# Performance work log

Measured on AMD Instinct MI355X. Metric: run time of the kernel, lower is better.

Reference implementation:

```python
import jax, jax.numpy as jnp
import numpy as np

MIN_BW = 0.1
MAX_BW = 10.0
BW_FACTOR = 1.0
SAMPLE = 512  # min(512, B) with B >= 512


def _pairwise_dist_sq(a, b):
    # ||a_i - b_j||^2 via GEMM: [N, M], avoids [N, M, D] intermediate
    a2 = jnp.sum(a * a, axis=-1)[:, None]
    b2 = jnp.sum(b * b, axis=-1)[None, :]
    d = a2 + b2 - 2.0 * (a @ b.T)
    return jnp.maximum(d, 0.0)


def _bandwidth(x, y):
    # torch: median heuristic on first SAMPLE rows, under no_grad
    xs = jax.lax.stop_gradient(x[:SAMPLE])
    ys = jax.lax.stop_gradient(y[:SAMPLE])
    dist_sq = _pairwise_dist_sq(xs, ys)
    bw_sq = jnp.median(dist_sq.reshape(-1))
    bw = jnp.sqrt(bw_sq / 2.0) * BW_FACTOR
    return jnp.clip(bw, MIN_BW, MAX_BW)


def setup_inputs() -> dict:
    key = jax.random.key(0)
    kx, ksx, ky, ksy = jax.random.split(key, 4)
    B, D = 4096, 512
    return {
        "x": jax.random.normal(kx, (B, D), dtype=jnp.float32),
        "score_x": jax.random.normal(ksx, (B, D), dtype=jnp.float32),
        "y": jax.random.normal(ky, (B, D), dtype=jnp.float32),
        "score_y": jax.random.normal(ksy, (B, D), dtype=jnp.float32),
    }


def reference(x, score_x, y, score_y):
    D = x.shape[-1]
    h = _bandwidth(x, y)
    h2 = h * h

    dist_sq = _pairwise_dist_sq(x, y)                      # [B, B]
    k = jnp.exp(-dist_sq / (2.0 * h2))                     # [B, B]

    # term1[i,j] = k[i,j] * <score_x_i, score_y_j>
    term1 = k * (score_x @ score_y.T)

    # term2[i,j] = <x_i - y_j, score_y_j> * k[i,j] / h^2
    term2 = ((x @ score_y.T) - jnp.sum(y * score_y, axis=-1)[None, :]) * k / h2

    # term3[i,j] = ||x_i - y_j||^2 * k / h^4 - k * D / h^2
    term3 = dist_sq * k / (h2 * h2) - k * (D / h2)

    return term1 + term2 + term3
```

## Files before the change

kernel.cpp:

```cpp
#include <hip/hip_runtime.h>
#include <hip/hip_bf16.h>

typedef __attribute__((ext_vector_type(8))) short bf16x8;
typedef __attribute__((ext_vector_type(4))) float f32x4;

#define B_N 4096
#define DIM 512
#define HBINS 8192

#define OFF_PARAMS 0
#define OFF_X2     256
#define OFF_Y2     16640
#define OFF_YSY    33024
#define OFF_HIST   49408
#define OFF_TILES  98304
#define MAT_ELEMS  2097152
#define WS_NEED    (OFF_TILES + (size_t)4 * MAT_ELEMS * 2)

static __device__ __forceinline__ unsigned short f2bf_rne(float f) {
    unsigned int u = __float_as_uint(f);
    u += 0x7FFFu + ((u >> 16) & 1u);
    return (unsigned short)(u >> 16);
}
static __device__ __forceinline__ float bf2f(unsigned short h) {
    return __uint_as_float(((unsigned int)h) << 16);
}

static __device__ __forceinline__ int swz(int r, int k) {
    return r * 32 + ((((k >> 3) ^ ((r >> 1) & 3))) << 3) + (k & 7);
}

__global__ __launch_bounds__(256) void k_hist2(
    const float* __restrict__ X, const float* __restrict__ Y,
    unsigned int* __restrict__ hist) {
    __shared__ __align__(16) unsigned short sA[2048];
    __shared__ __align__(16) unsigned short sB[2048];
    __shared__ unsigned int hloc[HBINS];
    __shared__ float x2s[64], y2s[64];

    int t = threadIdx.x;
    int bi = blockIdx.y, bj = blockIdx.x;
    for (int i = t; i < HBINS; i += 256) hloc[i] = 0;

    int lane = t & 63, w = t >> 6;
    int wm = w >> 1, wn = w & 1;
    int fr = lane & 15, fko = (lane >> 4) * 8;

    f32x4 axy[2][2];
#pragma unroll
    for (int i = 0; i < 2; ++i)
#pragma unroll
        for (int j = 0; j < 2; ++j) axy[i][j] = (f32x4)0.f;

    int r = t >> 2, k0 = (t & 3) * 8;
    const float* gx = X + (size_t)(bi * 64 + r) * DIM + k0;
    const float* gy = Y + (size_t)(bj * 64 + r) * DIM + k0;

    int ixA[2], ixB[2];
#pragma unroll
    for (int fm = 0; fm < 2; ++fm) ixA[fm] = swz(wm * 32 + fm * 16 + fr, fko);
#pragma unroll
    for (int fn = 0; fn < 2; ++fn) ixB[fn] = swz(wn * 32 + fn * 16 + fr, fko);

    float na = 0.f, nb = 0.f;
    float4 A0, A1, B0, B1;
#define LDK(kt_) do {                                                       \
        A0 = *(const float4*)(gx + (kt_) * 32);                             \
        A1 = *(const float4*)(gx + (kt_) * 32 + 4);                         \
        B0 = *(const float4*)(gy + (kt_) * 32);                             \
        B1 = *(const float4*)(gy + (kt_) * 32 + 4);                         \
    } while (0)

    LDK(0);
    for (int kt = 0; kt < 16; ++kt) {
        float av[8] = {A0.x, A0.y, A0.z, A0.w, A1.x, A1.y, A1.z, A1.w};
        float bv[8] = {B0.x, B0.y, B0.z, B0.w, B1.x, B1.y, B1.z, B1.w};
        bf16x8 ha, hb;
#pragma unroll
        for (int j = 0; j < 8; ++j) {
            na += av[j] * av[j];
            nb += bv[j] * bv[j];
            ha[j] = (short)f2bf_rne(av[j]);
            hb[j] = (short)f2bf_rne(bv[j]);
        }
        __syncthreads();
        *(bf16x8*)&sA[swz(r, k0)] = ha;
        *(bf16x8*)&sB[swz(r, k0)] = hb;
        if (kt < 15) LDK(kt + 1);
        __syncthreads();

        bf16x8 aX[2];
#pragma unroll
        for (int fm = 0; fm < 2; ++fm) aX[fm] = *(const bf16x8*)&sA[ixA[fm]];
#pragma unroll
        for (int fn = 0; fn < 2; ++fn) {
            bf16x8 bY = *(const bf16x8*)&sB[ixB[fn]];
#pragma unroll
            for (int fm = 0; fm < 2; ++fm)
                axy[fm][fn] = __builtin_amdgcn_mfma_f32_16x16x32_bf16(aX[fm], bY, axy[fm][fn], 0, 0, 0);
        }
    }
#undef LDK

    na += __shfl_xor(na, 1); na += __shfl_xor(na, 2);
    nb += __shfl_xor(nb, 1); nb += __shfl_xor(nb, 2);
    if ((t & 3) == 0) { x2s[r] = na; y2s[r] = nb; }
    __syncthreads();

    int fq = lane >> 4;
#pragma unroll
    for (int fm = 0; fm < 2; ++fm)
#pragma unroll
        for (int fn = 0; fn < 2; ++fn)
#pragma unroll
            for (int rr = 0; rr < 4; ++rr) {
                int rl = wm * 32 + fm * 16 + fq * 4 + rr;
                int cl = wn * 32 + fn * 16 + fr;
                float d = fmaxf(x2s[rl] + y2s[cl] - 2.0f * axy[fm][fn][rr], 0.0f);
                int bin = (int)(d * 4.0f);
                if (bin > HBINS - 1) bin = HBINS - 1;
                atomicAdd(&hloc[bin], 1u);
            }
    __syncthreads();
    for (int i = t; i < HBINS; i += 256) {
        unsigned int v = hloc[i];
        if (v) atomicAdd(&hist[i], v);
    }
}

__global__ __launch_bounds__(256, 1) void k_median(
    const unsigned int* __restrict__ hist, float* __restrict__ params) {
    __shared__ unsigned int hsum[HBINS];
    __shared__ unsigned int part[256];
    __shared__ float vv[2];
    int t = threadIdx.x;
    for (int i = t; i < HBINS / 4; i += 256)
        ((uint4*)hsum)[i] = ((const uint4*)hist)[i];
    __syncthreads();
    unsigned int s = 0;
#pragma unroll 8
    for (int b = t * 32; b < t * 32 + 32; ++b) s += hsum[b];
    part[t] = s;
    __syncthreads();
    unsigned int pre = 0;
    for (int i = 0; i < 256; ++i) {
        unsigned int v = part[i];
        if (i < t) pre += v;
    }
    const unsigned int kk1 = 131072u, kk2 = 131073u;
    unsigned int hi = pre + s;
#pragma unroll
    for (int sel = 0; sel < 2; ++sel) {
        unsigned int kk = sel ? kk2 : kk1;
        if (kk > pre && kk <= hi) {
            unsigned int cc = pre;
            for (int b = 0; b < 32; ++b) {
                cc += hsum[t * 32 + b];
                if (cc >= kk) { vv[sel] = ((float)(t * 32 + b) + 0.5f) * 0.25f; break; }
            }
        }
    }
    __syncthreads();
    if (t == 0) {
        float med = 0.5f * (vv[0] + vv[1]);
        float bw = sqrtf(med * 0.5f);
        bw = fminf(fmaxf(bw, 0.1f), 10.0f);
        float h2 = bw * bw;
        params[0] = 1.0f / (2.0f * h2);
        params[1] = 1.0f / h2;
        params[2] = 1.0f / (h2 * h2);
        params[3] = (float)DIM / h2;
    }
}

__global__ void k_prestats(const float* __restrict__ X, const float* __restrict__ SX,
                           const float* __restrict__ Y, const float* __restrict__ SY,
                           const float* __restrict__ params, unsigned short* __restrict__ tiles,
                           float* __restrict__ x2, float* __restrict__ y2,
                           float* __restrict__ ysy) {
    int side = blockIdx.z;
    const float* P = side ? Y : X;
    const float* Q = side ? SY : SX;
    float c1 = side ? 0.0f : params[1];
    int tile = blockIdx.x, t = threadIdx.x;
    unsigned short* base0 = tiles + (size_t)side * 2 * MAT_ELEMS;
    unsigned short* base1 = base0 + MAT_ELEMS;

#pragma unroll
    for (int kt2 = 0; kt2 < 2; ++kt2) {
        int kt = blockIdx.y * 2 + kt2;
        unsigned short* d0 = base0 + (size_t)(tile * 16 + kt) * 4096;
        unsigned short* d1 = base1 + (size_t)(tile * 16 + kt) * 4096;

#pragma unroll
        for (int c = 0; c < 2; ++c) {
            int u = c * 256 + t;
            int r = u >> 2;
            int k = (((u & 3) ^ ((u >> 3) & 3))) << 3;
            const float* gp = P + (size_t)(tile * 128 + r) * DIM + kt * 32 + k;
            float4 p0 = *(const float4*)gp;
            float4 p1 = *(const float4*)(gp + 4);
            float pv[8] = {p0.x, p0.y, p0.z, p0.w, p1.x, p1.y, p1.z, p1.w};
            float s1 = 0.f, s2 = 0.f;
            bf16x8 h0;
            if (side) {
                const float* gq = Q + (size_t)(tile * 128 + r) * DIM + kt * 32 + k;
                float4 q0 = *(const float4*)gq;
                float4 q1 = *(const float4*)(gq + 4);
                float qv[8] = {q0.x, q0.y, q0.z, q0.w, q1.x, q1.y, q1.z, q1.w};
#pragma unroll
                for (int j = 0; j < 8; ++j) {
                    s1 += pv[j] * pv[j];
                    s2 += pv[j] * qv[j];
                    h0[j] = (short)f2bf_rne(pv[j]);
                }
            } else {
#pragma unroll
                for (int j = 0; j < 8; ++j) {
                    s1 += pv[j] * pv[j];
                    h0[j] = (short)f2bf_rne(pv[j]);
                }
            }
            *(bf16x8*)&d0[u * 8] = h0;
            s1 += __shfl_xor(s1, 1); s1 += __shfl_xor(s1, 2);
            if (side) { s2 += __shfl_xor(s2, 1); s2 += __shfl_xor(s2, 2); }
            if ((t & 3) == 0) {
                int row = tile * 128 + r;
                if (side == 0) {
                    atomicAdd(&x2[row], s1);
                } else {
                    atomicAdd(&y2[row], s1);
                    atomicAdd(&ysy[row], s2);
                }
            }
        }

#pragma unroll
        for (int c = 0; c < 2; ++c) {
            int v = c * 256 + t;
            int r = (v >> 6) * 16 + (v & 15);
            int k = ((v >> 4) & 3) << 3;
            const float* gq = Q + (size_t)(tile * 128 + r) * DIM + kt * 32 + k;
            float4 q0 = *(const float4*)gq;
            float4 q1 = *(const float4*)(gq + 4);
            float qv[8] = {q0.x, q0.y, q0.z, q0.w, q1.x, q1.y, q1.z, q1.w};
            bf16x8 h1;
            if (side == 0) {
                const float* gp = P + (size_t)(tile * 128 + r) * DIM + kt * 32 + k;
                float4 p0 = *(const float4*)gp;
                float4 p1 = *(const float4*)(gp + 4);
                float pv[8] = {p0.x, p0.y, p0.z, p0.w, p1.x, p1.y, p1.z, p1.w};
#pragma unroll
                for (int j = 0; j < 8; ++j) h1[j] = (short)f2bf_rne(qv[j] + c1 * pv[j]);
            } else {
#pragma unroll
                for (int j = 0; j < 8; ++j) h1[j] = (short)f2bf_rne(qv[j]);
            }
            *(bf16x8*)&d1[v * 8] = h1;
        }
    }
}

#define GLD(g, l) __builtin_amdgcn_global_load_lds(                                   \
    (const __attribute__((address_space(1))) void*)(g),                               \
    (__attribute__((address_space(3))) void*)(l), 16, 0, 0)

__global__ __launch_bounds__(256, 2) void k_main(
    const unsigned short* __restrict__ tiles,
    const float* __restrict__ x2g, const float* __restrict__ y2g,
    const float* __restrict__ ysyg, const float* __restrict__ params,
    float* __restrict__ out) {
    __shared__ __align__(16) unsigned short sA[2][4096];
    __shared__ __align__(16) unsigned short sB[2][4096];
    __shared__ float x2s[128], y2s[128], ysys[128];

    int t = threadIdx.x;
    int bm = blockIdx.y, bn = blockIdx.x;
    if (t < 128) x2s[t] = x2g[bm * 128 + t];
    else { y2s[t - 128] = y2g[bn * 128 + (t - 128)]; ysys[t - 128] = ysyg[bn * 128 + (t - 128)]; }
    __syncthreads();

    int lane = t & 63, w = t >> 6;
    int wm = w >> 1, wn = w & 1;
    int fr = lane & 15, fko = (lane >> 4) * 8;

    f32x4 axy[4][4], acb[4][4];
#pragma unroll
    for (int i = 0; i < 4; ++i)
#pragma unroll
        for (int j = 0; j < 4; ++j) { axy[i][j] = (f32x4)0.f; acb[i][j] = (f32x4)0.f; }

    const unsigned short* gaX = tiles + (size_t)(bm * 16) * 4096 + t * 8;
    const unsigned short* gbY = tiles + (size_t)2 * MAT_ELEMS + (size_t)(bn * 16) * 4096 + t * 8;
    const unsigned short* gaC = tiles + (size_t)MAT_ELEMS + (size_t)(bm * 16) * 4096
                              + (wm * 4) * 512 + lane * 8;
    const unsigned short* gbS = tiles + (size_t)3 * MAT_ELEMS + (size_t)(bn * 16) * 4096
                              + (wn * 4) * 512 + lane * 8;

#define STAGE(buf, kt_) do {                                                     \
        const unsigned short* pa_ = gaX + (size_t)(kt_) * 4096;                  \
        const unsigned short* pb_ = gbY + (size_t)(kt_) * 4096;                  \
        GLD(pa_,        &sA[buf][t * 8]);                                        \
        GLD(pa_ + 2048, &sA[buf][2048 + t * 8]);                                 \
        GLD(pb_,        &sB[buf][t * 8]);                                        \
        GLD(pb_ + 2048, &sB[buf][2048 + t * 8]);                                 \
    } while (0)

#define FRAGLD(dC, dS, kt_) do {                                                 \
        const unsigned short* pc_ = gaC + (size_t)(kt_) * 4096;                  \
        const unsigned short* ps_ = gbS + (size_t)(kt_) * 4096;                  \
        dC[0] = *(const bf16x8*)(pc_);        dS[0] = *(const bf16x8*)(ps_);     \
        dC[1] = *(const bf16x8*)(pc_ + 512);  dS[1] = *(const bf16x8*)(ps_ + 512);\
        dC[2] = *(const bf16x8*)(pc_ + 1024); dS[2] = *(const bf16x8*)(ps_ + 1024);\
        dC[3] = *(const bf16x8*)(pc_ + 1536); dS[3] = *(const bf16x8*)(ps_ + 1536);\
    } while (0)

    int ixA[4], ixB[4];
#pragma unroll
    for (int fm = 0; fm < 4; ++fm) ixA[fm] = swz(wm * 64 + fm * 16 + fr, fko);
#pragma unroll
    for (int fn = 0; fn < 4; ++fn) ixB[fn] = swz(wn * 64 + fn * 16 + fr, fko);

    bf16x8 fC0[4], fS0[4], fC1[4], fS1[4];

#define KSTEP(CB, CURC, CURS, NXTC, NXTS, NKT, DOPF) do {                        \
        asm volatile("s_waitcnt vmcnt(8)" ::: "memory");   \
        __builtin_amdgcn_sched_barrier(0);                                       \
        __builtin_amdgcn_s_barrier();                                            \
        __builtin_amdgcn_sched_barrier(0);                                       \
        if (DOPF) {                                                              \
            STAGE(CB ^ 1, NKT);                                                  \
            FRAGLD(NXTC, NXTS, NKT);                                             \
        }                                                                        \
        bf16x8 dX[4], dY[4];                                                     \
        dX[0] = *(const bf16x8*)&sA[CB][ixA[0]];                                 \
        dX[1] = *(const bf16x8*)&sA[CB][ixA[1]];                                 \
        dX[2] = *(const bf16x8*)&sA[CB][ixA[2]];                                 \
        dX[3] = *(const bf16x8*)&sA[CB][ixA[3]];                                 \
        dY[0] = *(const bf16x8*)&sB[CB][ixB[0]];                                 \
        dY[1] = *(const bf16x8*)&sB[CB][ixB[1]];                                 \
        dY[2] = *(const bf16x8*)&sB[CB][ixB[2]];                                 \
        dY[3] = *(const bf16x8*)&sB[CB][ixB[3]];                                 \
        __builtin_amdgcn_s_setprio(1);                                           \
        _Pragma("unroll")                                                        \
        for (int fn_ = 0; fn_ < 4; ++fn_) {                                      \
            _Pragma("unroll")                                                    \
            for (int fm_ = 0; fm_ < 4; ++fm_) {                                  \
                axy[fm_][fn_] = __builtin_amdgcn_mfma_f32_16x16x32_bf16(         \
                    dX[fm_], dY[fn_], axy[fm_][fn_], 0, 0, 0);                   \
                acb[fm_][fn_] = __builtin_amdgcn_mfma_f32_16x16x32_bf16(         \
                    CURC[fm_], CURS[fn_], acb[fm_][fn_], 0, 0, 0);               \
            }                                                                    \
        }                                                                        \
        __builtin_amdgcn_s_setprio(0);                                           \
        __builtin_amdgcn_sched_barrier(0);                                       \
    } while (0)

    STAGE(0, 0);
    FRAGLD(fC0, fS0, 0);

    for (int k2 = 0; k2 < 7; ++k2) {
        KSTEP(0, fC0, fS0, fC1, fS1, 2 * k2 + 1, 1);
        KSTEP(1, fC1, fS1, fC0, fS0, 2 * k2 + 2, 1);
    }
    KSTEP(0, fC0, fS0, fC1, fS1, 15, 1);
    KSTEP(1, fC1, fS1, fC0, fS0, 0, 0);
#undef KSTEP
#undef STAGE
#undef FRAGLD

    float c0 = params[0], c1 = params[1], c2 = params[2], c3 = params[3];
    int fq = lane >> 4;
#pragma unroll
    for (int fm = 0; fm < 4; ++fm) {
#pragma unroll
        for (int fn = 0; fn < 4; ++fn) {
#pragma unroll
            for (int r = 0; r < 4; ++r) {
                int rl = wm * 64 + fm * 16 + fq * 4 + r;
                int cl = wn * 64 + fn * 16 + fr;
                float d = fmaxf(x2s[rl] + y2s[cl] - 2.0f * axy[fm][fn][r], 0.0f);
                float kv = __expf(-d * c0);
                out[(size_t)(bm * 128 + rl) * B_N + (bn * 128 + cl)] =
                    kv * (acb[fm][fn][r] - c1 * ysys[cl] + d * c2 - c3);
            }
        }
    }
}

__global__ void k_rowstats(const float* __restrict__ X, const float* __restrict__ Y,
                           const float* __restrict__ SY,
                           float* __restrict__ x2, float* __restrict__ y2,
                           float* __restrict__ ysy) {
    int t = threadIdx.x;
    int r = blockIdx.x * 4 + (t >> 6);
    int lane = t & 63;
    const float4* px = (const float4*)(X + (size_t)r * DIM) + lane * 2;
    const float4* py = (const float4*)(Y + (size_t)r * DIM) + lane * 2;
    const float4* ps = (const float4*)(SY + (size_t)r * DIM) + lane * 2;
    float4 a0 = px[0], a1 = px[1];
    float4 b0 = py[0], b1 = py[1];
    float4 c0 = ps[0], c1 = ps[1];
    float s1 = a0.x*a0.x + a0.y*a0.y + a0.z*a0.z + a0.w*a0.w
             + a1.x*a1.x + a1.y*a1.y + a1.z*a1.z + a1.w*a1.w;
    float s2 = b0.x*b0.x + b0.y*b0.y + b0.z*b0.z + b0.w*b0.w
             + b1.x*b1.x + b1.y*b1.y + b1.z*b1.z + b1.w*b1.w;
    float s3 = b0.x*c0.x + b0.y*c0.y + b0.z*c0.z + b0.w*c0.w
             + b1.x*c1.x + b1.y*c1.y + b1.z*c1.z + b1.w*c1.w;
#pragma unroll
    for (int o = 32; o > 0; o >>= 1) {
        s1 += __shfl_down(s1, o);
        s2 += __shfl_down(s2, o);
        s3 += __shfl_down(s3, o);
    }
    if (lane == 0) { x2[r] = s1; y2[r] = s2; ysy[r] = s3; }
}

__global__ void k_hist_fp32(const float* __restrict__ X, const float* __restrict__ Y,
                            const float* __restrict__ x2, const float* __restrict__ y2,
                            unsigned int* __restrict__ hist) {
    __shared__ float xs[32][68];
    __shared__ float ys[32][68];
    __shared__ unsigned int hloc[HBINS];
    int t = threadIdx.x;
    for (int i = t; i < HBINS; i += 256) hloc[i] = 0;
    int i0 = blockIdx.y * 32, j0 = blockIdx.x * 32;
    float a00 = 0.f, a01 = 0.f, a10 = 0.f, a11 = 0.f;
    int ti = (t >> 4) * 2, tj = (t & 15) * 2;
    for (int c = 0; c < 8; ++c) {
        __syncthreads();
        int rr = t >> 3, cc = (t & 7) * 8;
        const float* gx = X + (size_t)(i0 + rr) * DIM + c * 64 + cc;
        *(float4*)&xs[rr][cc] = *(const float4*)gx;
        *(float4*)&xs[rr][cc + 4] = *(const float4*)(gx + 4);
        const float* gy = Y + (size_t)(j0 + rr) * DIM + c * 64 + cc;
        *(float4*)&ys[rr][cc] = *(const float4*)gy;
        *(float4*)&ys[rr][cc + 4] = *(const float4*)(gy + 4);
        __syncthreads();
        for (int kk = 0; kk < 64; ++kk) {
            float a0 = xs[ti][kk], a1 = xs[ti + 1][kk];
            float b0 = ys[tj][kk], b1 = ys[tj + 1][kk];
            a00 += a0 * b0; a01 += a0 * b1; a10 += a1 * b0; a11 += a1 * b1;
        }
    }
    float s[2][2] = {{a00, a01}, {a10, a11}};
#pragma unroll
    for (int ii = 0; ii < 2; ++ii)
#pragma unroll
        for (int jj = 0; jj < 2; ++jj) {
            float d = fmaxf(x2[i0 + ti + ii] + y2[j0 + tj + jj] - 2.f * s[ii][jj], 0.f);
            int bin = (int)(d * 4.0f);
            if (bin > HBINS - 1) bin = HBINS - 1;
            atomicAdd(&hloc[bin], 1u);
        }
    __syncthreads();
    for (int i = t; i < HBINS; i += 256) {
        unsigned int v = hloc[i];
        if (v) atomicAdd(&hist[i], v);
    }
}

static __device__ __forceinline__ void store_hi(unsigned short* tile, int r, int k0,
                                                float4 v0, float4 v1) {
    bf16x8 h;
    h[0] = (short)f2bf_rne(v0.x); h[1] = (short)f2bf_rne(v0.y);
    h[2] = (short)f2bf_rne(v0.z); h[3] = (short)f2bf_rne(v0.w);
    h[4] = (short)f2bf_rne(v1.x); h[5] = (short)f2bf_rne(v1.y);
    h[6] = (short)f2bf_rne(v1.z); h[7] = (short)f2bf_rne(v1.w);
    *(bf16x8*)&tile[swz(r, k0)] = h;
}
static __device__ __forceinline__ void store_hilo(unsigned short* th, unsigned short* tl,
                                                  int r, int k0, float4 v0, float4 v1) {
    float f[8] = {v0.x, v0.y, v0.z, v0.w, v1.x, v1.y, v1.z, v1.w};
    bf16x8 h, l;
#pragma unroll
    for (int j = 0; j < 8; ++j) {
        unsigned short hh = f2bf_rne(f[j]);
        h[j] = (short)hh;
        l[j] = (short)f2bf_rne(f[j] - bf2f(hh));
    }
    *(bf16x8*)&th[swz(r, k0)] = h;
    *(bf16x8*)&tl[swz(r, k0)] = l;
}

__global__ __launch_bounds__(256, 2) void k_main_fb(
    const float* __restrict__ X, const float* __restrict__ SX,
    const float* __restrict__ Y, const float* __restrict__ SY,
    const float* __restrict__ x2g, const float* __restrict__ y2g,
    const float* __restrict__ ysyg, const float* __restrict__ params,
    float* __restrict__ out) {
    __shared__ __align__(16) unsigned short tX[4096];
    __shared__ __align__(16) unsigned short tSXH[4096];
    __shared__ __align__(16) unsigned short tSXL[4096];
    __shared__ __align__(16) unsigned short tY[2048];
    __shared__ __align__(16) unsigned short tSYH[2048];
    __shared__ __align__(16) unsigned short tSYL[2048];
    __shared__ float x2s[128];
    __shared__ float y2s[64];
    __shared__ float ysys[64];

    int t = threadIdx.x;
    int bm = blockIdx.y, bn = blockIdx.x;
    if (t < 128) x2s[t] = x2g[bm * 128 + t];
    else if (t < 192) y2s[t - 128] = y2g[bn * 64 + (t - 128)];
    else ysys[t - 192] = ysyg[bn * 64 + (t - 192)];

    int lane = t & 63, w = t >> 6, wm = w >> 1, wn = w & 1;
    f32x4 axy[4][2], ass[4][2], axsy[4][2];
#pragma unroll
    for (int i = 0; i < 4; ++i)
#pragma unroll
        for (int j = 0; j < 2; ++j) {
            axy[i][j] = (f32x4)0.f; ass[i][j] = (f32x4)0.f; axsy[i][j] = (f32x4)0.f;
        }

    for (int kt = 0; kt < DIM / 32; ++kt) {
        int kb = kt * 32;
#pragma unroll
        for (int h = 0; h < 2; ++h) {
            int s = t + h * 256;
            int r = s >> 2, k0 = (s & 3) * 8;
            const float* gx = X + (size_t)(bm * 128 + r) * DIM + kb + k0;
            store_hi(tX, r, k0, *(const float4*)gx, *(const float4*)(gx + 4));
            const float* gs = SX + (size_t)(bm * 128 + r) * DIM + kb + k0;
            store_hilo(tSXH, tSXL, r, k0, *(const float4*)gs, *(const float4*)(gs + 4));
        }
        {
            int r = t >> 2, k0 = (t & 3) * 8;
            const float* gy = Y + (size_t)(bn * 64 + r) * DIM + kb + k0;
            store_hi(tY, r, k0, *(const float4*)gy, *(const float4*)(gy + 4));
            const float* gq = SY + (size_t)(bn * 64 + r) * DIM + kb + k0;
            store_hilo(tSYH, tSYL, r, k0, *(const float4*)gq, *(const float4*)(gq + 4));
        }
        __syncthreads();

        int fr = lane & 15, fk = (lane >> 4) * 8;
        bf16x8 aX[4], aSH[4], aSL[4];
#pragma unroll
        for (int fm = 0; fm < 4; ++fm) {
            int ix = swz(wm * 64 + fm * 16 + fr, fk);
            aX[fm] = *(const bf16x8*)&tX[ix];
            aSH[fm] = *(const bf16x8*)&tSXH[ix];
            aSL[fm] = *(const bf16x8*)&tSXL[ix];
        }
#pragma unroll
        for (int fn = 0; fn < 2; ++fn) {
            int iy = swz(wn * 32 + fn * 16 + fr, fk);
            bf16x8 bY = *(const bf16x8*)&tY[iy];
            bf16x8 bH = *(const bf16x8*)&tSYH[iy];
            bf16x8 bL = *(const bf16x8*)&tSYL[iy];
#pragma unroll
            for (int fm = 0; fm < 4; ++fm) {
                axy[fm][fn] = __builtin_amdgcn_mfma_f32_16x16x32_bf16(aX[fm], bY, axy[fm][fn], 0, 0, 0);
                ass[fm][fn] = __builtin_amdgcn_mfma_f32_16x16x32_bf16(aSH[fm], bH, ass[fm][fn], 0, 0, 0);
                ass[fm][fn] = __builtin_amdgcn_mfma_f32_16x16x32_bf16(aSH[fm], bL, ass[fm][fn], 0, 0, 0);
                ass[fm][fn] = __builtin_amdgcn_mfma_f32_16x16x32_bf16(aSL[fm], bH, ass[fm][fn], 0, 0, 0);
                axsy[fm][fn] = __builtin_amdgcn_mfma_f32_16x16x32_bf16(aX[fm], bH, axsy[fm][fn], 0, 0, 0);
            }
        }
        __syncthreads();
    }

    float c0 = params[0], c1 = params[1], c2 = params[2], c3 = params[3];
    int fr = lane & 15, fq = lane >> 4;
#pragma unroll
    for (int fm = 0; fm < 4; ++fm)
#pragma unroll
        for (int fn = 0; fn < 2; ++fn)
#pragma unroll
            for (int r = 0; r < 4; ++r) {
                int rl = wm * 64 + fm * 16 + fq * 4 + r;
                int cl = wn * 32 + fn * 16 + fr;
                float d = fmaxf(x2s[rl] + y2s[cl] - 2.0f * axy[fm][fn][r], 0.0f);
                float kv = __expf(-d * c0);
                out[(size_t)(bm * 128 + rl) * B_N + (bn * 64 + cl)] =
                    kv * ass[fm][fn][r] + (axsy[fm][fn][r] - ysys[cl]) * (kv * c1)
                    + d * kv * c2 - kv * c3;
            }
}

extern "C" void kernel_launch(void* const* d_in, const int* in_sizes, int n_in,
                              void* d_out, int out_size, void* d_ws, size_t ws_size,
                              hipStream_t stream) {
    const float* x  = (const float*)d_in[0];
    const float* sx = (const float*)d_in[1];
    const float* y  = (const float*)d_in[2];
    const float* sy = (const float*)d_in[3];
    float* out = (float*)d_out;
    char* ws = (char*)d_ws;
    float* params = (float*)(ws + OFF_PARAMS);
    float* x2 = (float*)(ws + OFF_X2);
    float* y2 = (float*)(ws + OFF_Y2);
    float* ysy = (float*)(ws + OFF_YSY);
    unsigned int* hist = (unsigned int*)(ws + OFF_HIST);
    unsigned short* tiles = (unsigned short*)(ws + OFF_TILES);

    if (ws_size >= WS_NEED) {
        hipMemsetAsync(ws + OFF_X2, 0, 3 * 16384 + HBINS * 4, stream);
        k_hist2<<<dim3(8, 8), dim3(256), 0, stream>>>(x, y, hist);
        k_median<<<1, 256, 0, stream>>>(hist, params);
        k_prestats<<<dim3(32, 8, 2), dim3(256), 0, stream>>>(x, sx, y, sy, params, tiles,
                                                             x2, y2, ysy);
        k_main<<<dim3(32, 32), dim3(256), 0, stream>>>(tiles, x2, y2, ysy, params, out);
    } else {
        hipMemsetAsync(hist, 0, HBINS * 4, stream);
        k_rowstats<<<B_N / 4, 256, 0, stream>>>(x, y, sy, x2, y2, ysy);
        k_hist_fp32<<<dim3(16, 16), dim3(256), 0, stream>>>(x, y, x2, y2, hist);
        k_median<<<1, 256, 0, stream>>>(hist, params);
        k_main_fb<<<dim3(64, 32), dim3(256), 0, stream>>>(x, sx, y, sy, x2, y2, ysy, params, out);
    }
}
```

Baseline: 85.48 us.

## Merge histogram, median and param-independent preprocessing into one kernel

Folds the histogram kernel, the median kernel and the param-independent part of the tile preprocessing (bf16 conversion of X, Y and SY plus row norms) into a single 576-block launch. The last block to finish, detected with an atomic counter, computes the median. Only the param-dependent SX+c1*X tile conversion stays in a small separate kernel. Tile storage moves to a fragment-linear layout, so the main kernel uses plain lane*8 offsets instead of swizzled indices. This removes two launches and lets the preprocessing run alongside the histogram, at the cost of a threadfence/counter tail and uneven block work.

New measurement: 146.8 us. 71.7% more time.

```diff
diff --git a/kernel.cpp b/kernel.cpp
--- a/kernel.cpp
+++ b/kernel.cpp
@@ -13,9 +13,11 @@
 #define OFF_Y2     16640
 #define OFF_YSY    33024
 #define OFF_HIST   49408
+#define OFF_CNT    82176
 #define OFF_TILES  98304
 #define MAT_ELEMS  2097152
 #define WS_NEED    (OFF_TILES + (size_t)4 * MAT_ELEMS * 2)
+#define MEMSET_LEN 82180
 
 static __device__ __forceinline__ unsigned short f2bf_rne(float f) {
     unsigned int u = __float_as_uint(f);
@@ -30,232 +32,246 @@
     return r * 32 + ((((k >> 3) ^ ((r >> 1) & 3))) << 3) + (k & 7);
 }
 
-__global__ __launch_bounds__(256) void k_hist2(
+
+__global__ __launch_bounds__(256) void k_pre1(
     const float* __restrict__ X, const float* __restrict__ Y,
-    unsigned int* __restrict__ hist) {
-    __shared__ __align__(16) unsigned short sA[2048];
-    __shared__ __align__(16) unsigned short sB[2048];
+    const float* __restrict__ SY, unsigned short* __restrict__ tiles,
+    float* __restrict__ x2, float* __restrict__ y2, float* __restrict__ ysy,
+    unsigned int* __restrict__ hist, unsigned int* __restrict__ cnt,
+    float* __restrict__ params) {
+    __shared__ __align__(16) unsigned short sAB[4096];
     __shared__ unsigned int hloc[HBINS];
-    __shared__ float x2s[64], y2s[64];
-
-    int t = threadIdx.x;
-    int bi = blockIdx.y, bj = blockIdx.x;
-    for (int i = t; i < HBINS; i += 256) hloc[i] = 0;
-
-    int lane = t & 63, w = t >> 6;
-    int wm = w >> 1, wn = w & 1;
-    int fr = lane & 15, fko = (lane >> 4) * 8;
-
-    f32x4 axy[2][2];
-#pragma unroll
-    for (int i = 0; i < 2; ++i)
-#pragma unroll
-        for (int j = 0; j < 2; ++j) axy[i][j] = (f32x4)0.f;
-
-    int r = t >> 2, k0 = (t & 3) * 8;
-    const float* gx = X + (size_t)(bi * 64 + r) * DIM + k0;
-    const float* gy = Y + (size_t)(bj * 64 + r) * DIM + k0;
-
-    int ixA[2], ixB[2];
-#pragma unroll
-    for (int fm = 0; fm < 2; ++fm) ixA[fm] = swz(wm * 32 + fm * 16 + fr, fko);
-#pragma unroll
-    for (int fn = 0; fn < 2; ++fn) ixB[fn] = swz(wn * 32 + fn * 16 + fr, fko);
-
-    float na = 0.f, nb = 0.f;
-    float4 A0, A1, B0, B1;
-#define LDK(kt_) do {                                                       \
-        A0 = *(const float4*)(gx + (kt_) * 32);                             \
-        A1 = *(const float4*)(gx + (kt_) * 32 + 4);                         \
-        B0 = *(const float4*)(gy + (kt_) * 32);                             \
-        B1 = *(const float4*)(gy + (kt_) * 32 + 4);                         \
-    } while (0)
-
-    LDK(0);
-    for (int kt = 0; kt < 16; ++kt) {
-        float av[8] = {A0.x, A0.y, A0.z, A0.w, A1.x, A1.y, A1.z, A1.w};
-        float bv[8] = {B0.x, B0.y, B0.z, B0.w, B1.x, B1.y, B1.z, B1.w};
-        bf16x8 ha, hb;
-#pragma unroll
-        for (int j = 0; j < 8; ++j) {
-            na += av[j] * av[j];
-            nb += bv[j] * bv[j];
-            ha[j] = (short)f2bf_rne(av[j]);
-            hb[j] = (short)f2bf_rne(bv[j]);
-        }
-        __syncthreads();
-        *(bf16x8*)&sA[swz(r, k0)] = ha;
-        *(bf16x8*)&sB[swz(r, k0)] = hb;
-        if (kt < 15) LDK(kt + 1);
-        __syncthreads();
-
-        bf16x8 aX[2];
-#pragma unroll
-        for (int fm = 0; fm < 2; ++fm) aX[fm] = *(const bf16x8*)&sA[ixA[fm]];
-#pragma unroll
-        for (int fn = 0; fn < 2; ++fn) {
-            bf16x8 bY = *(const bf16x8*)&sB[ixB[fn]];
-#pragma unroll
-            for (int fm = 0; fm < 2; ++fm)
-                axy[fm][fn] = __builtin_amdgcn_mfma_f32_16x16x32_bf16(aX[fm], bY, axy[fm][fn], 0, 0, 0);
-        }
-    }
-#undef LDK
-
-    na += __shfl_xor(na, 1); na += __shfl_xor(na, 2);
-    nb += __shfl_xor(nb, 1); nb += __shfl_xor(nb, 2);
-    if ((t & 3) == 0) { x2s[r] = na; y2s[r] = nb; }
-    __syncthreads();
-
-    int fq = lane >> 4;
-#pragma unroll
-    for (int fm = 0; fm < 2; ++fm)
-#pragma unroll
-        for (int fn = 0; fn < 2; ++fn)
-#pragma unroll
-            for (int rr = 0; rr < 4; ++rr) {
-                int rl = wm * 32 + fm * 16 + fq * 4 + rr;
-                int cl = wn * 32 + fn * 16 + fr;
-                float d = fmaxf(x2s[rl] + y2s[cl] - 2.0f * axy[fm][fn][rr], 0.0f);
-                int bin = (int)(d * 4.0f);
-                if (bin > HBINS - 1) bin = HBINS - 1;
-                atomicAdd(&hloc[bin], 1u);
-            }
-    __syncthreads();
-    for (int i = t; i < HBINS; i += 256) {
-        unsigned int v = hloc[i];
-        if (v) atomicAdd(&hist[i], v);
-    }
-}
-
-__global__ __launch_bounds__(256, 1) void k_median(
-    const unsigned int* __restrict__ hist, float* __restrict__ params) {
-    __shared__ unsigned int hsum[HBINS];
+    __shared__ float rn[128];
     __shared__ unsigned int part[256];
     __shared__ float vv[2];
-    int t = threadIdx.x;
-    for (int i = t; i < HBINS / 4; i += 256)
-        ((uint4*)hsum)[i] = ((const uint4*)hist)[i];
+    __shared__ unsigned int lastFlag;
+
+    int b = blockIdx.x, t = threadIdx.x;
+
+    if (b < 512) {
+        int side = b >> 8;
+        int tile = (b & 255) >> 3;
+        int ky = b & 7;
+        unsigned short* base0 = tiles + (size_t)side * 2 * MAT_ELEMS;
+        unsigned short* base1 = base0 + MAT_ELEMS;
+#pragma unroll
+        for (int kt2 = 0; kt2 < 2; ++kt2) {
+            int kt = ky * 2 + kt2;
+            unsigned short* d0 = base0 + (size_t)(tile * 16 + kt) * 4096;
+            unsigned short* d1 = base1 + (size_t)(tile * 16 + kt) * 4096;
+#pragma unroll
+            for (int c = 0; c < 2; ++c) {
+                int v = c * 256 + t;
+                int r = (v >> 6) * 16 + (v & 15);
+                int k = ((v >> 4) & 3) << 3;
+                const float* gp = (side ? Y : X) + (size_t)(tile * 128 + r) * DIM + kt * 32 + k;
+                float4 p0 = *(const float4*)gp;
+                float4 p1 = *(const float4*)(gp + 4);
+                float pv[8] = {p0.x, p0.y, p0.z, p0.w, p1.x, p1.y, p1.z, p1.w};
+                float s1 = 0.f, s2 = 0.f;
+                bf16x8 h0;
+                if (side) {
+                    const float* gq = SY + (size_t)(tile * 128 + r) * DIM + kt * 32 + k;
+                    float4 q0 = *(const float4*)gq;
+                    float4 q1 = *(const float4*)(gq + 4);
+                    float qv[8] = {q0.x, q0.y, q0.z, q0.w, q1.x, q1.y, q1.z, q1.w};
+                    bf16x8 h1;
+#pragma unroll
+                    for (int j = 0; j < 8; ++j) {
+                        s1 += pv[j] * pv[j];
+                        s2 += pv[j] * qv[j];
+                        h0[j] = (short)f2bf_rne(pv[j]);
+                        h1[j] = (short)f2bf_rne(qv[j]);
+                    }
+                    *(bf16x8*)&d1[v * 8] = h1;
+                } else {
+#pragma unroll
+                    for (int j = 0; j < 8; ++j) {
+                        s1 += pv[j] * pv[j];
+                        h0[j] = (short)f2bf_rne(pv[j]);
+                    }
+                }
+                *(bf16x8*)&d0[v * 8] = h0;
+                s1 += __shfl_xor(s1, 16); s1 += __shfl_xor(s1, 32);
+                if (side) { s2 += __shfl_xor(s2, 16); s2 += __shfl_xor(s2, 32); }
+                if ((t & 48) == 0) {
+                    int row = tile * 128 + r;
+                    if (side == 0) {
+                        atomicAdd(&x2[row], s1);
+                    } else {
+                        atomicAdd(&y2[row], s1);
+                        atomicAdd(&ysy[row], s2);
+                    }
+                }
+            }
+        }
+    } else {
+        unsigned short* sA = &sAB[0];
+        unsigned short* sB = &sAB[2048];
+        float* x2s = &rn[0];
+        float* y2s = &rn[64];
+        int hb = b - 512;
+        int bi = hb >> 3, bj = hb & 7;
+        for (int i = t; i < HBINS; i += 256) hloc[i] = 0;
+
+        int lane = t & 63, w = t >> 6;
+        int wm = w >> 1, wn = w & 1;
+        int fr = lane & 15, fko = (lane >> 4) * 8;
+
+        f32x4 axy[2][2];
+#pragma unroll
+        for (int i = 0; i < 2; ++i)
+#pragma unroll
+            for (int j = 0; j < 2; ++j) axy[i][j] = (f32x4)0.f;
+
+        int r = t >> 2, k0 = (t & 3) * 8;
+        const float* gx = X + (size_t)(bi * 64 + r) * DIM + k0;
+        const float* gy = Y + (size_t)(bj * 64 + r) * DIM + k0;
+
+        int ixA[2], ixB[2];
+#pragma unroll
+        for (int fm = 0; fm < 2; ++fm) ixA[fm] = swz(wm * 32 + fm * 16 + fr, fko);
+#pragma unroll
+        for (int fn = 0; fn < 2; ++fn) ixB[fn] = swz(wn * 32 + fn * 16 + fr, fko);
+
+        float na = 0.f, nb = 0.f;
+        float4 A0, A1, B0, B1;
+#define LDK(kt_) do {                                                       \
+            A0 = *(const float4*)(gx + (kt_) * 32);                         \
+            A1 = *(const float4*)(gx + (kt_) * 32 + 4);                     \
+            B0 = *(const float4*)(gy + (kt_) * 32);                         \
+            B1 = *(const float4*)(gy + (kt_) * 32 + 4);                     \
+        } while (0)
+
+        LDK(0);
+        for (int kt = 0; kt < 16; ++kt) {
+            float av[8] = {A0.x, A0.y, A0.z, A0.w, A1.x, A1.y, A1.z, A1.w};
+            float bv[8] = {B0.x, B0.y, B0.z, B0.w, B1.x, B1.y, B1.z, B1.w};
+            bf16x8 ha, hb2;
+#pragma unroll
+            for (int j = 0; j < 8; ++j) {
+                na += av[j] * av[j];
+                nb += bv[j] * bv[j];
+                ha[j] = (short)f2bf_rne(av[j]);
+                hb2[j] = (short)f2bf_rne(bv[j]);
+            }
+            __syncthreads();
+            *(bf16x8*)&sA[swz(r, k0)] = ha;
+            *(bf16x8*)&sB[swz(r, k0)] = hb2;
+            if (kt < 15) LDK(kt + 1);
+            __syncthreads();
+
+            bf16x8 aX[2];
+#pragma unroll
+            for (int fm = 0; fm < 2; ++fm) aX[fm] = *(const bf16x8*)&sA[ixA[fm]];
+#pragma unroll
+            for (int fn = 0; fn < 2; ++fn) {
+                bf16x8 bY = *(const bf16x8*)&sB[ixB[fn]];
+#pragma unroll
+                for (int fm = 0; fm < 2; ++fm)
+                    axy[fm][fn] = __builtin_amdgcn_mfma_f32_16x16x32_bf16(aX[fm], bY, axy[fm][fn], 0, 0, 0);
+            }
+        }
+#undef LDK
+
+        na += __shfl_xor(na, 1); na += __shfl_xor(na, 2);
+        nb += __shfl_xor(nb, 1); nb += __shfl_xor(nb, 2);
+        if ((t & 3) == 0) { x2s[r] = na; y2s[r] = nb; }
+        __syncthreads();
+
+        int fq = lane >> 4;
+#pragma unroll
+        for (int fm = 0; fm < 2; ++fm)
+#pragma unroll
+            for (int fn = 0; fn < 2; ++fn)
+#pragma unroll
+                for (int rr = 0; rr < 4; ++rr) {
+                    int rl = wm * 32 + fm * 16 + fq * 4 + rr;
+                    int cl = wn * 32 + fn * 16 + fr;
+                    float d = fmaxf(x2s[rl] + y2s[cl] - 2.0f * axy[fm][fn][rr], 0.0f);
+                    int bin = (int)(d * 4.0f);
+                    if (bin > HBINS - 1) bin = HBINS - 1;
+                    atomicAdd(&hloc[bin], 1u);
+                }
+        __syncthreads();
+        for (int i = t; i < HBINS; i += 256) {
+            unsigned int v = hloc[i];
+            if (v) atomicAdd(&hist[i], v);
+        }
+    }
+
+    __threadfence();
     __syncthreads();
-    unsigned int s = 0;
+    if (t == 0) lastFlag = (atomicAdd(cnt, 1u) == 575u);
+    __syncthreads();
+    if (lastFlag) {
+        __threadfence();
+        for (int i = t; i < HBINS / 4; i += 256)
+            ((uint4*)hloc)[i] = ((const uint4*)hist)[i];
+        __syncthreads();
+        unsigned int s = 0;
 #pragma unroll 8
-    for (int b = t * 32; b < t * 32 + 32; ++b) s += hsum[b];
-    part[t] = s;
-    __syncthreads();
-    unsigned int pre = 0;
-    for (int i = 0; i < 256; ++i) {
-        unsigned int v = part[i];
-        if (i < t) pre += v;
-    }
-    const unsigned int kk1 = 131072u, kk2 = 131073u;
-    unsigned int hi = pre + s;
-#pragma unroll
-    for (int sel = 0; sel < 2; ++sel) {
-        unsigned int kk = sel ? kk2 : kk1;
-        if (kk > pre && kk <= hi) {
-            unsigned int cc = pre;
-            for (int b = 0; b < 32; ++b) {
-                cc += hsum[t * 32 + b];
-                if (cc >= kk) { vv[sel] = ((float)(t * 32 + b) + 0.5f) * 0.25f; break; }
-            }
-        }
-    }
-    __syncthreads();
-    if (t == 0) {
-        float med = 0.5f * (vv[0] + vv[1]);
-        float bw = sqrtf(med * 0.5f);
-        bw = fminf(fmaxf(bw, 0.1f), 10.0f);
-        float h2 = bw * bw;
-        params[0] = 1.0f / (2.0f * h2);
-        params[1] = 1.0f / h2;
-        params[2] = 1.0f / (h2 * h2);
-        params[3] = (float)DIM / h2;
-    }
-}
-
-__global__ void k_prestats(const float* __restrict__ X, const float* __restrict__ SX,
-                           const float* __restrict__ Y, const float* __restrict__ SY,
-                           const float* __restrict__ params, unsigned short* __restrict__ tiles,
-                           float* __restrict__ x2, float* __restrict__ y2,
-                           float* __restrict__ ysy) {
-    int side = blockIdx.z;
-    const float* P = side ? Y : X;
-    const float* Q = side ? SY : SX;
-    float c1 = side ? 0.0f : params[1];
+        for (int bb = t * 32; bb < t * 32 + 32; ++bb) s += hloc[bb];
+        part[t] = s;
+        __syncthreads();
+        unsigned int pre = 0;
+        for (int i = 0; i < 256; ++i) {
+            unsigned int v = part[i];
+            if (i < t) pre += v;
+        }
+        const unsigned int kk1 = 131072u, kk2 = 131073u;
+        unsigned int hi = pre + s;
+#pragma unroll
+        for (int sel = 0; sel < 2; ++sel) {
+            unsigned int kk = sel ? kk2 : kk1;
+            if (kk > pre && kk <= hi) {
+                unsigned int cc = pre;
+                for (int bb = 0; bb < 32; ++bb) {
+                    cc += hloc[t * 32 + bb];
+                    if (cc >= kk) { vv[sel] = ((float)(t * 32 + bb) + 0.5f) * 0.25f; break; }
+                }
+            }
+        }
+        __syncthreads();
+        if (t == 0) {
+            float med = 0.5f * (vv[0] + vv[1]);
+            float bw = sqrtf(med * 0.5f);
+            bw = fminf(fmaxf(bw, 0.1f), 10.0f);
+            float h2 = bw * bw;
+            params[0] = 1.0f / (2.0f * h2);
+            params[1] = 1.0f / h2;
+            params[2] = 1.0f / (h2 * h2);
+            params[3] = (float)DIM / h2;
+        }
+    }
+}
+
+__global__ __launch_bounds__(256) void k_preC(
+    const float* __restrict__ X, const float* __restrict__ SX,
+    const float* __restrict__ params, unsigned short* __restrict__ tiles) {
+    float c1 = params[1];
     int tile = blockIdx.x, t = threadIdx.x;
-    unsigned short* base0 = tiles + (size_t)side * 2 * MAT_ELEMS;
-    unsigned short* base1 = base0 + MAT_ELEMS;
-
+    unsigned short* base1 = tiles + MAT_ELEMS;
 #pragma unroll
     for (int kt2 = 0; kt2 < 2; ++kt2) {
         int kt = blockIdx.y * 2 + kt2;
-        unsigned short* d0 = base0 + (size_t)(tile * 16 + kt) * 4096;
         unsigned short* d1 = base1 + (size_t)(tile * 16 + kt) * 4096;
-
-#pragma unroll
-        for (int c = 0; c < 2; ++c) {
-            int u = c * 256 + t;
-            int r = u >> 2;
-            int k = (((u & 3) ^ ((u >> 3) & 3))) << 3;
-            const float* gp = P + (size_t)(tile * 128 + r) * DIM + kt * 32 + k;
-            float4 p0 = *(const float4*)gp;
-            float4 p1 = *(const float4*)(gp + 4);
-            float pv[8] = {p0.x, p0.y, p0.z, p0.w, p1.x, p1.y, p1.z, p1.w};
-            float s1 = 0.f, s2 = 0.f;
-            bf16x8 h0;
-            if (side) {
-                const float* gq = Q + (size_t)(tile * 128 + r) * DIM + kt * 32 + k;
-                float4 q0 = *(const float4*)gq;
-                float4 q1 = *(const float4*)(gq + 4);
-                float qv[8] = {q0.x, q0.y, q0.z, q0.w, q1.x, q1.y, q1.z, q1.w};
-#pragma unroll
-                for (int j = 0; j < 8; ++j) {
-                    s1 += pv[j] * pv[j];
-                    s2 += pv[j] * qv[j];
-                    h0[j] = (short)f2bf_rne(pv[j]);
-                }
-            } else {
-#pragma unroll
-                for (int j = 0; j < 8; ++j) {
-                    s1 += pv[j] * pv[j];
-                    h0[j] = (short)f2bf_rne(pv[j]);
-                }
-            }
-            *(bf16x8*)&d0[u * 8] = h0;
-            s1 += __shfl_xor(s1, 1); s1 += __shfl_xor(s1, 2);
-            if (side) { s2 += __shfl_xor(s2, 1); s2 += __shfl_xor(s2, 2); }
-            if ((t & 3) == 0) {
-                int row = tile * 128 + r;
-                if (side == 0) {
-                    atomicAdd(&x2[row], s1);
-                } else {
-                    atomicAdd(&y2[row], s1);
-                    atomicAdd(&ysy[row], s2);
-                }
-            }
-        }
-
 #pragma unroll
         for (int c = 0; c < 2; ++c) {
             int v = c * 256 + t;
             int r = (v >> 6) * 16 + (v & 15);
             int k = ((v >> 4) & 3) << 3;
-            const float* gq = Q + (size_t)(tile * 128 + r) * DIM + kt * 32 + k;
+            const float* gp = X + (size_t)(tile * 128 + r) * DIM + kt * 32 + k;
+            const float* gq = SX + (size_t)(tile * 128 + r) * DIM + kt * 32 + k;
+            float4 p0 = *(const float4*)gp;
+            float4 p1 = *(const float4*)(gp + 4);
             float4 q0 = *(const float4*)gq;
             float4 q1 = *(const float4*)(gq + 4);
+            float pv[8] = {p0.x, p0.y, p0.z, p0.w, p1.x, p1.y, p1.z, p1.w};
             float qv[8] = {q0.x, q0.y, q0.z, q0.w, q1.x, q1.y, q1.z, q1.w};
             bf16x8 h1;
-            if (side == 0) {
-                const float* gp = P + (size_t)(tile * 128 + r) * DIM + kt * 32 + k;
-                float4 p0 = *(const float4*)gp;
-                float4 p1 = *(const float4*)(gp + 4);
-                float pv[8] = {p0.x, p0.y, p0.z, p0.w, p1.x, p1.y, p1.z, p1.w};
-#pragma unroll
-                for (int j = 0; j < 8; ++j) h1[j] = (short)f2bf_rne(qv[j] + c1 * pv[j]);
-            } else {
-#pragma unroll
-                for (int j = 0; j < 8; ++j) h1[j] = (short)f2bf_rne(qv[j]);
-            }
+#pragma unroll
+            for (int j = 0; j < 8; ++j) h1[j] = (short)f2bf_rne(qv[j] + c1 * pv[j]);
             *(bf16x8*)&d1[v * 8] = h1;
         }
     }
@@ -282,7 +298,6 @@
 
     int lane = t & 63, w = t >> 6;
     int wm = w >> 1, wn = w & 1;
-    int fr = lane & 15, fko = (lane >> 4) * 8;
 
     f32x4 axy[4][4], acb[4][4];
 #pragma unroll
@@ -317,9 +332,9 @@
 
     int ixA[4], ixB[4];
 #pragma unroll
-    for (int fm = 0; fm < 4; ++fm) ixA[fm] = swz(wm * 64 + fm * 16 + fr, fko);
-#pragma unroll
-    for (int fn = 0; fn < 4; ++fn) ixB[fn] = swz(wn * 64 + fn * 16 + fr, fko);
+    for (int fm = 0; fm < 4; ++fm) ixA[fm] = (wm * 4 + fm) * 512 + lane * 8;
+#pragma unroll
+    for (int fn = 0; fn < 4; ++fn) ixB[fn] = (wn * 4 + fn) * 512 + lane * 8;
 
     bf16x8 fC0[4], fS0[4], fC1[4], fS1[4];
 
@@ -370,7 +385,7 @@
 #undef FRAGLD
 
     float c0 = params[0], c1 = params[1], c2 = params[2], c3 = params[3];
-    int fq = lane >> 4;
+    int fr = lane & 15, fq = lane >> 4;
 #pragma unroll
     for (int fm = 0; fm < 4; ++fm) {
 #pragma unroll
@@ -460,6 +475,51 @@
     }
 }
 
+__global__ __launch_bounds__(256, 1) void k_median(
+    const unsigned int* __restrict__ hist, float* __restrict__ params) {
+    __shared__ unsigned int hsum[HBINS];
+    __shared__ unsigned int part[256];
+    __shared__ float vv[2];
+    int t = threadIdx.x;
+    for (int i = t; i < HBINS / 4; i += 256)
+        ((uint4*)hsum)[i] = ((const uint4*)hist)[i];
+    __syncthreads();
+    unsigned int s = 0;
+#pragma unroll 8
+    for (int b = t * 32; b < t * 32 + 32; ++b) s += hsum[b];
+    part[t] = s;
+    __syncthreads();
+    unsigned int pre = 0;
+    for (int i = 0; i < 256; ++i) {
+        unsigned int v = part[i];
+        if (i < t) pre += v;
+    }
+    const unsigned int kk1 = 131072u, kk2 = 131073u;
+    unsigned int hi = pre + s;
+#pragma unroll
+    for (int sel = 0; sel < 2; ++sel) {
+        unsigned int kk = sel ? kk2 : kk1;
+        if (kk > pre && kk <= hi) {
+            unsigned int cc = pre;
+            for (int b = 0; b < 32; ++b) {
+                cc += hsum[t * 32 + b];
+                if (cc >= kk) { vv[sel] = ((float)(t * 32 + b) + 0.5f) * 0.25f; break; }
+            }
+        }
+    }
+    __syncthreads();
+    if (t == 0) {
+        float med = 0.5f * (vv[0] + vv[1]);
+        float bw = sqrtf(med * 0.5f);
+        bw = fminf(fmaxf(bw, 0.1f), 10.0f);
+        float h2 = bw * bw;
+        params[0] = 1.0f / (2.0f * h2);
+        params[1] = 1.0f / h2;
+        params[2] = 1.0f / (h2 * h2);
+        params[3] = (float)DIM / h2;
+    }
+}
+
 static __device__ __forceinline__ void store_hi(unsigned short* tile, int r, int k0,
                                                 float4 v0, float4 v1) {
     bf16x8 h;
@@ -593,14 +653,13 @@
     float* y2 = (float*)(ws + OFF_Y2);
     float* ysy = (float*)(ws + OFF_YSY);
     unsigned int* hist = (unsigned int*)(ws + OFF_HIST);
+    unsigned int* cnt = (unsigned int*)(ws + OFF_CNT);
     unsigned short* tiles = (unsigned short*)(ws + OFF_TILES);
 
     if (ws_size >= WS_NEED) {
-        hipMemsetAsync(ws + OFF_X2, 0, 3 * 16384 + HBINS * 4, stream);
-        k_hist2<<<dim3(8, 8), dim3(256), 0, stream>>>(x, y, hist);
-        k_median<<<1, 256, 0, stream>>>(hist, params);
-        k_prestats<<<dim3(32, 8, 2), dim3(256), 0, stream>>>(x, sx, y, sy, params, tiles,
-                                                             x2, y2, ysy);
+        hipMemsetAsync(ws, 0, MEMSET_LEN, stream);
+        k_pre1<<<576, 256, 0, stream>>>(x, y, sy, tiles, x2, y2, ysy, hist, cnt, params);
+        k_preC<<<dim3(32, 8), 256, 0, stream>>>(x, sx, params, tiles);
         k_main<<<dim3(32, 32), dim3(256), 0, stream>>>(tiles, x2, y2, ysy, params, out);
     } else {
         hipMemsetAsync(hist, 0, HBINS * 4, stream);
```
